# Kernel optimization log

Hardware: AMD Instinct MI355X
Metric: run time of the kernel (lower is better)

## Reference

```python
import jax, jax.numpy as jnp
import numpy as np

N = 100000
E = 3200000

def spmm(edge_row, edge_col, edge_val, support):
    # out[i] = sum_{(i,j) in edges} w_ij * support[j]
    gathered = support[edge_col] * edge_val[:, None]  # [E, F]
    return jax.ops.segment_sum(gathered, edge_row, num_segments=N)

def setup_inputs() -> dict:
    key = jax.random.key(0)
    ks = jax.random.split(key, 10)
    x = jax.random.normal(ks[0], (N, 512), dtype=jnp.float32)
    edge_row = jax.random.randint(ks[1], (E,), 0, N, dtype=jnp.int32)
    edge_col = jax.random.randint(ks[2], (E,), 0, N, dtype=jnp.int32)
    edge_val = jax.random.uniform(ks[3], (E,), dtype=jnp.float32) / 32.0  # ~normalized adj
    def glorot_like(k, shape):
        stdv = 1.0 / np.sqrt(shape[-1])
        return jax.random.uniform(k, shape, dtype=jnp.float32, minval=-stdv, maxval=stdv)
    W1 = glorot_like(ks[4], (512, 256)); b1 = glorot_like(ks[5], (256,))
    W2 = glorot_like(ks[6], (256, 256)); b2 = glorot_like(ks[7], (256,))
    W3 = glorot_like(ks[8], (256, 64)); b3 = glorot_like(ks[9], (64,))
    return {"x": x, "edge_row": edge_row, "edge_col": edge_col, "edge_val": edge_val,
            "W1": W1, "b1": b1, "W2": W2, "b2": b2, "W3": W3, "b3": b3}

def reference(x, edge_row, edge_col, edge_val, W1, b1, W2, b2, W3, b3):
    # layer 1: mm + spmm + bias + relu
    h = spmm(edge_row, edge_col, edge_val, x @ W1) + b1
    h = jax.nn.relu(h)
    # hidden layer (layer_num=3 -> one hidden GraphConvolution); dropout is inference no-op
    h = spmm(edge_row, edge_col, edge_val, h @ W2) + b2
    h = jax.nn.relu(h)
    # output layer
    h = spmm(edge_row, edge_col, edge_val, h @ W3) + b3
    # task='nodecls', ppi=False
    return jax.nn.log_softmax(h, axis=1)
```

## Files before the change

kernel.cpp:

```cpp
#include <hip/hip_runtime.h>
#include <stdint.h>
#include <stddef.h>

typedef __bf16 bf16x8 __attribute__((ext_vector_type(8)));
typedef float  f32x4  __attribute__((ext_vector_type(4)));
typedef float  f32x2  __attribute__((ext_vector_type(2)));

static __device__ __forceinline__ float bf2f(unsigned short u) {
    union { unsigned int i; float f; } v; v.i = ((unsigned int)u) << 16; return v.f;
}
static __device__ __forceinline__ unsigned short f2bf(float f) {
    union { float f; unsigned int i; } v; v.f = f;
    unsigned int r = v.i + 0x7FFFu + ((v.i >> 16) & 1u);
    return (unsigned short)(r >> 16);
}
static __device__ __forceinline__ unsigned cvt_pk_bf16(float a, float b) {
    unsigned r;
    asm volatile("v_cvt_pk_bf16_f32 %0, %1, %2" : "=v"(r) : "v"(a), "v"(b));
    return r;
}
static __device__ __forceinline__ unsigned char f2fp8(float f) {
    return (unsigned char)(__builtin_amdgcn_cvt_pk_fp8_f32(f, f, 0, false) & 0xFF);
}

#define N_NODES 100000
#define N_EDGES 3200000
#define MPAD    100096
#define NB      782
#define NBLK    256
#define EB      (N_EDGES / NBLK)
#define COLMASK 0xFFFFF


__global__ __launch_bounds__(256) void bucket_hist(const int* __restrict__ er, int* __restrict__ blockCnt) {
    __shared__ int h[NB];
    for (int i = threadIdx.x; i < NB; i += 256) h[i] = 0;
    __syncthreads();
    int base = blockIdx.x * EB;
    for (int e = base + threadIdx.x; e < base + EB; e += 256)
        atomicAdd(&h[er[e] >> 7], 1);
    __syncthreads();
    for (int i = threadIdx.x; i < NB; i += 256) blockCnt[blockIdx.x * NB + i] = h[i];
}

__global__ __launch_bounds__(256) void bucket_scan_a(const int* __restrict__ blockCnt,
                                                     int* __restrict__ blockOff,
                                                     int* __restrict__ bucketTotal) {
    __shared__ int s[256];
    int b = blockIdx.x, t = threadIdx.x;
    int v = blockCnt[t * NB + b];
    s[t] = v; __syncthreads();
    for (int off = 1; off < 256; off <<= 1) {
        int u = (t >= off) ? s[t - off] : 0;
        __syncthreads();
        s[t] += u;
        __syncthreads();
    }
    blockOff[t * NB + b] = s[t] - v;
    if (t == 255) bucketTotal[b] = s[255];
}

__global__ __launch_bounds__(1024) void bucket_scan_b(const int* __restrict__ bucketTotal,
                                                      int* __restrict__ bucketStart,
                                                      int* __restrict__ rp, int E,
                                                      int2* __restrict__ cpad) {
    __shared__ int s[1024];
    int t = threadIdx.x;
    int v = (t < NB) ? bucketTotal[t] : 0;
    s[t] = v; __syncthreads();
    for (int off = 1; off < 1024; off <<= 1) {
        int u = (t >= off) ? s[t - off] : 0;
        __syncthreads();
        s[t] += u;
        __syncthreads();
    }
    if (t < NB) bucketStart[t] = s[t] - v;
    if (t == 0) {
        bucketStart[NB] = E; rp[N_NODES] = E;
        for (int i = 0; i < 16; i++) cpad[i] = make_int2(0, 0);
    }
}

__global__ __launch_bounds__(1024) void bucket_scatter(const int* __restrict__ er, const int* __restrict__ ec,
                                                       const float* __restrict__ ev,
                                                       const int* __restrict__ blkCnt,
                                                       const int* __restrict__ blockOff,
                                                       const int* __restrict__ bucketStart,
                                                       int2* __restrict__ cpackT) {
    __shared__ int2 buf[EB];
    __shared__ int  s[1024];
    __shared__ int  scanB[NB];
    __shared__ int  cur[NB];
    int t = threadIdx.x;
    int v = (t < NB) ? blkCnt[blockIdx.x * NB + t] : 0;
    s[t] = v; __syncthreads();
    for (int off = 1; off < 1024; off <<= 1) {
        int u = (t >= off) ? s[t - off] : 0;
        __syncthreads();
        s[t] += u;
        __syncthreads();
    }
    if (t < NB) { scanB[t] = s[t] - v; cur[t] = s[t] - v; }
    __syncthreads();
    int base = blockIdx.x * EB;
    for (int e = base + t; e < base + EB; e += 1024) {
        int r = er[e];
        int p = atomicAdd(&cur[r >> 7], 1);
        buf[p] = make_int2(((r & 127) << 20) | ec[e], __float_as_int(ev[e]));
    }
    __syncthreads();
    for (int i = t; i < EB; i += 1024) {
        int lo = 0, hi = NB - 1;
        while (lo < hi) { int mid = (lo + hi) >> 1; if (cur[mid] <= i) lo = mid + 1; else hi = mid; }
        int gpos = bucketStart[lo] + blockOff[blockIdx.x * NB + lo] + (i - scanB[lo]);
        cpackT[gpos] = buf[i];
    }
}

__global__ __launch_bounds__(256) void bucket_sort(const int2* __restrict__ cpackT,
                                                   const int* __restrict__ bucketStart,
                                                   int2* __restrict__ cpack, int* __restrict__ rp) {
    __shared__ int cnt[128];
    __shared__ int cursor[128];
    int b = blockIdx.x, t = threadIdx.x;
    int s = bucketStart[b], e = bucketStart[b + 1];
    if (t < 128) cnt[t] = 0;
    __syncthreads();
    for (int j = s + t; j < e; j += 256)
        atomicAdd(&cnt[cpackT[j].x >> 20], 1);
    __syncthreads();
    int val = (t < 128) ? cnt[t] : 0;
    for (int off = 1; off < 128; off <<= 1) {
        int u = (t < 128 && t >= off) ? cnt[t - off] : 0;
        __syncthreads();
        if (t < 128) cnt[t] += u;
        __syncthreads();
    }
    if (t < 128) {
        int excl = cnt[t] - val;
        cursor[t] = s + excl;
        int gr = b * 128 + t;
        if (gr < N_NODES) rp[gr] = s + excl;
    }
    __syncthreads();
    for (int j = s + t; j < e; j += 256) {
        int2 v = cpackT[j];
        int p = atomicAdd(&cursor[v.x >> 20], 1);
        cpack[p] = make_int2((v.x & COLMASK) << 8, v.y);
    }
}

__global__ __launch_bounds__(256) void transpose_all(const float* __restrict__ W1, unsigned short* __restrict__ Wt1,
                                                     const float* __restrict__ W2, unsigned short* __restrict__ Wt2,
                                                     const float* __restrict__ W3, unsigned short* __restrict__ Wt3) {
    int i = blockIdx.x * 256 + threadIdx.x;
    const int S1 = 512 * 256, S2 = 256 * 256, S3 = 256 * 64;
    if (i < S1) {
        int k = i / 256, n = i % 256;
        Wt1[(size_t)n * 512 + k] = f2bf(W1[i]);
    } else if (i < S1 + S2) {
        int j = i - S1; int k = j / 256, n = j % 256;
        Wt2[(size_t)n * 256 + k] = f2bf(W2[j]);
    } else if (i < S1 + S2 + S3) {
        int j = i - S1 - S2; int k = j / 64, n = j % 64;
        Wt3[(size_t)n * 256 + k] = f2bf(W3[j]);
    }
}

template<int BM, int BN, int BK, int WROWS, int WCOLS, bool A_F32, int OUT>
__global__ __launch_bounds__(WROWS* WCOLS * 64) void gemm_mfma(const void* __restrict__ Aptr,
                                                 const unsigned short* __restrict__ Bt,
                                                 void* __restrict__ Cptr,
                                                 int K, int Nc, int Mclamp) {
    constexpr int THREADS = WROWS * WCOLS * 64;
    constexpr int WM = BM / WROWS, WN = BN / WCOLS;
    constexpr int MT = WM / 16, NT = WN / 16;
    constexpr int LDA = BK + 8;
    constexpr int KV = BK / 8;

    __shared__ unsigned short lds_a[BM * LDA];
    __shared__ unsigned short lds_b[BN * LDA];

    const int tid  = threadIdx.x;
    const int wid  = tid >> 6, lane = tid & 63;
    const int wrow = wid / WCOLS, wcol = wid % WCOLS;
    const int bm = blockIdx.x * BM, bn = blockIdx.y * BN;
    const int r = lane & 15, q = lane >> 4;

    const float*          Af = (const float*)Aptr;
    const unsigned short* Ab = (const unsigned short*)Aptr;

    f32x4 acc[MT][NT];
    f32x4 zero = {0.f, 0.f, 0.f, 0.f};
#pragma unroll
    for (int mi = 0; mi < MT; mi++)
#pragma unroll
        for (int ni = 0; ni < NT; ni++) acc[mi][ni] = zero;

    for (int k0 = 0; k0 < K; k0 += BK) {
#pragma unroll
        for (int it = 0; it < (BM * KV) / THREADS; it++) {
            int v = tid + it * THREADS;
            int row = v / KV, kc = (v % KV) * 8;
            int grow = bm + row;
            uint4 d;
            if constexpr (A_F32) {
                grow = (grow <= Mclamp) ? grow : Mclamp;
                const float4* pp = (const float4*)(Af + (size_t)grow * K + k0 + kc);
                float4 f0 = pp[0], f1 = pp[1];
                d.x = cvt_pk_bf16(f0.x, f0.y);
                d.y = cvt_pk_bf16(f0.z, f0.w);
                d.z = cvt_pk_bf16(f1.x, f1.y);
                d.w = cvt_pk_bf16(f1.z, f1.w);
            } else {
                d = *(const uint4*)(Ab + (size_t)grow * K + k0 + kc);
            }
            *(uint4*)&lds_a[row * LDA + kc] = d;
        }
#pragma unroll
        for (int it = 0; it < (BN * KV) / THREADS; it++) {
            int v = tid + it * THREADS;
            int row = v / KV, kc = (v % KV) * 8;
            uint4 d = *(const uint4*)(Bt + (size_t)(bn + row) * K + k0 + kc);
            *(uint4*)&lds_b[row * LDA + kc] = d;
        }
        __syncthreads();

#pragma unroll
        for (int kk = 0; kk < BK; kk += 32) {
            bf16x8 av[MT], bv[NT];
#pragma unroll
            for (int mi = 0; mi < MT; mi++)
                av[mi] = *(const bf16x8*)&lds_a[(wrow * WM + mi * 16 + r) * LDA + kk + q * 8];
#pragma unroll
            for (int ni = 0; ni < NT; ni++)
                bv[ni] = *(const bf16x8*)&lds_b[(wcol * WN + ni * 16 + r) * LDA + kk + q * 8];
#pragma unroll
            for (int mi = 0; mi < MT; mi++)
#pragma unroll
                for (int ni = 0; ni < NT; ni++)
                    acc[mi][ni] = __builtin_amdgcn_mfma_f32_16x16x32_bf16(av[mi], bv[ni], acc[mi][ni], 0, 0, 0);
        }
        __syncthreads();
    }

#pragma unroll
    for (int mi = 0; mi < MT; mi++) {
        int row = bm + wrow * WM + mi * 16 + q * 4;
#pragma unroll
        for (int ni = 0; ni < NT; ni++) {
            int cc = bn + wcol * WN + ni * 16 + r;
#pragma unroll
            for (int d = 0; d < 4; d++) {
                if constexpr (OUT == 0) {
                    ((unsigned short*)Cptr)[(size_t)(row + d) * Nc + cc] = f2bf(acc[mi][ni][d]);
                } else {
                    ((unsigned char*)Cptr)[(size_t)(row + d) * Nc + cc] = f2fp8(acc[mi][ni][d]);
                }
            }
        }
    }
}

__global__ __launch_bounds__(256) void spmm_f256_fp8(const int* __restrict__ rp, const int2* __restrict__ cpack,
                                                     const unsigned char* __restrict__ Z8,
                                                     const float* __restrict__ bias, unsigned short* __restrict__ H, int N) {
    int w = __builtin_amdgcn_readfirstlane((int)((blockIdx.x * 256 + threadIdx.x) >> 6));
    if (w >= N) return;
    int lane = threadIdx.x & 63;
    int f4 = lane * 4;
    int s = __builtin_amdgcn_readfirstlane(rp[w]);
    int e = __builtin_amdgcn_readfirstlane(rp[w + 1]);
    f32x2 acc01 = {0.f, 0.f}, acc23 = {0.f, 0.f};
    int j = s;

#define EDGE_BLK(UN, MASKED) { \
        int2 eb[UN]; \
        _Pragma("unroll") \
        for (int t = 0; t < UN; t++) eb[t] = cpack[j + t]; \
        _Pragma("unroll") \
        for (int t = 0; t < UN; t++) { \
            int ex = __builtin_amdgcn_readfirstlane(eb[t].x); \
            int ew = __builtin_amdgcn_readfirstlane(eb[t].y); \
            if (MASKED) ew = (j + t < e) ? ew : 0; \
            float wt = __int_as_float(ew); \
            unsigned z = *(const unsigned*)(Z8 + (size_t)(unsigned)ex + f4); \
            f32x2 lo = __builtin_amdgcn_cvt_pk_f32_fp8((int)z, false); \
            f32x2 hi = __builtin_amdgcn_cvt_pk_f32_fp8((int)z, true);  \
            f32x2 wv = {wt, wt}; \
            acc01 += wv * lo; \
            acc23 += wv * hi; \
        } }

    for (; j + 16 <= e; j += 16) EDGE_BLK(16, false)
    for (; j < e; j += 8)        EDGE_BLK(8,  true)
#undef EDGE_BLK

    float4 b = *(const float4*)(bias + f4);
    float a0 = fmaxf(acc01.x + b.x, 0.f), a1 = fmaxf(acc01.y + b.y, 0.f);
    float a2 = fmaxf(acc23.x + b.z, 0.f), a3 = fmaxf(acc23.y + b.w, 0.f);
    ushort4 o; o.x = f2bf(a0); o.y = f2bf(a1); o.z = f2bf(a2); o.w = f2bf(a3);
    *(ushort4*)(H + (size_t)w * 256 + f4) = o;
}

__global__ __launch_bounds__(256) void spmm_f64_lsm(const int* __restrict__ rp, const int2* __restrict__ cpack,
                                                    const unsigned short* __restrict__ Z,
                                                    const float* __restrict__ bias, float* __restrict__ out, int N) {
    int w = __builtin_amdgcn_readfirstlane((int)((blockIdx.x * 256 + threadIdx.x) >> 6));
    if (w >= N) return;
    int lane = threadIdx.x & 63;
    const unsigned char* Zb = (const unsigned char*)Z;
    int s = __builtin_amdgcn_readfirstlane(rp[w]);
    int e = __builtin_amdgcn_readfirstlane(rp[w + 1]);
    float acc = 0.f;
    int j = s;

#define EDGE_BLK(UN, MASKED) { \
        int2 eb[UN]; \
        _Pragma("unroll") \
        for (int t = 0; t < UN; t++) eb[t] = cpack[j + t]; \
        _Pragma("unroll") \
        for (int t = 0; t < UN; t++) { \
            int ex = __builtin_amdgcn_readfirstlane(eb[t].x); \
            int ew = __builtin_amdgcn_readfirstlane(eb[t].y); \
            if (MASKED) ew = (j + t < e) ? ew : 0; \
            float wt = __int_as_float(ew); \
             \
            unsigned short z = *(const unsigned short*)(Zb + (size_t)(unsigned)(ex >> 1) + lane * 2); \
            acc += wt * bf2f(z); \
        } }

    for (; j + 8 <= e; j += 8) EDGE_BLK(8, false)
    for (; j < e; j += 4)      EDGE_BLK(4, true)
#undef EDGE_BLK

    float a = acc + bias[lane];
    float m = a;
#pragma unroll
    for (int off = 32; off >= 1; off >>= 1) m = fmaxf(m, __shfl_xor(m, off, 64));
    float p = __expf(a - m);
    float sum = p;
#pragma unroll
    for (int off = 32; off >= 1; off >>= 1) sum += __shfl_xor(sum, off, 64);
    out[(size_t)w * 64 + lane] = a - m - __logf(sum);
}

extern "C" void kernel_launch(void* const* d_in, const int* in_sizes, int n_in,
                              void* d_out, int out_size, void* d_ws, size_t ws_size,
                              hipStream_t stream) {
    const float* x  = (const float*)d_in[0];
    const int*   er = (const int*)  d_in[1];
    const int*   ec = (const int*)  d_in[2];
    const float* ev = (const float*)d_in[3];
    const float* W1 = (const float*)d_in[4];
    const float* b1 = (const float*)d_in[5];
    const float* W2 = (const float*)d_in[6];
    const float* b2 = (const float*)d_in[7];
    const float* W3 = (const float*)d_in[8];
    const float* b3 = (const float*)d_in[9];

    const int N = N_NODES, E = N_EDGES;

    char* p = (char*)d_ws;
    auto alloc = [&](size_t bytes) -> char* {
        char* q = p; p += (bytes + 255) & ~(size_t)255; return q;
    };
    unsigned short* Wt1    = (unsigned short*)alloc((size_t)256 * 512 * 2);
    unsigned short* Wt2    = (unsigned short*)alloc((size_t)256 * 256 * 2);
    unsigned short* Wt3    = (unsigned short*)alloc((size_t)64  * 256 * 2);
    int*            rp     = (int*)  alloc((size_t)(N + 1) * 4);
    int*            blkCnt = (int*)  alloc((size_t)NBLK * NB * 4);
    int*            blkOff = (int*)  alloc((size_t)NBLK * NB * 4);
    int*            bktTot = (int*)  alloc((size_t)NB * 4);
    int*            bktSt  = (int*)  alloc((size_t)(NB + 1) * 4);
    int2*           cpack  = (int2*) alloc((size_t)(E + 16) * 8);
    unsigned char*  Z8     = (unsigned char*) alloc((size_t)MPAD * 256);
    unsigned short* bufA   = (unsigned short*)alloc((size_t)MPAD * 256 * 2);
    unsigned short* bufB   = (unsigned short*)alloc((size_t)MPAD * 256 * 2);
    int2*           cpackT = (int2*)bufA;

    bucket_hist   <<<NBLK, 256, 0, stream>>>(er, blkCnt);
    bucket_scan_a <<<NB,   256, 0, stream>>>(blkCnt, blkOff, bktTot);
    bucket_scan_b <<<1,   1024, 0, stream>>>(bktTot, bktSt, rp, E, cpack + E);
    bucket_scatter<<<NBLK, 1024, 0, stream>>>(er, ec, ev, blkCnt, blkOff, bktSt, cpackT);
    bucket_sort   <<<NB,   256, 0, stream>>>(cpackT, bktSt, cpack, rp);

    transpose_all<<<(512*256 + 256*256 + 256*64 + 255) / 256, 256, 0, stream>>>(W1, Wt1, W2, Wt2, W3, Wt3);

    gemm_mfma<128, 128, 64, 4, 2, true , 1><<<dim3(MPAD / 128, 2), 512, 0, stream>>>(x,    Wt1, Z8,   512, 256, N - 1);
    spmm_f256_fp8<<<N / 4, 256, 0, stream>>>(rp, cpack, Z8, b1, bufB, N);
    gemm_mfma<128, 128, 64, 4, 2, false, 1><<<dim3(MPAD / 128, 2), 512, 0, stream>>>(bufB, Wt2, Z8,   256, 256, N - 1);
    spmm_f256_fp8<<<N / 4, 256, 0, stream>>>(rp, cpack, Z8, b2, bufB, N);
    gemm_mfma<128, 64, 64, 4, 2, false, 0><<<dim3(MPAD / 128, 1), 512, 0, stream>>>(bufB, Wt3, bufA, 256, 64, N - 1);
    spmm_f64_lsm<<<N / 4, 256, 0, stream>>>(rp, cpack, bufA, b3, (float*)d_out, N);
}
```

Measured before the change: 788.6 us.

## Register-prefetch next GEMM tile during MFMA and widen SpMM edge unroll

```diff
diff --git a/kernel.cpp b/kernel.cpp
--- a/kernel.cpp
+++ b/kernel.cpp
@@ -177,6 +177,8 @@
     constexpr int MT = WM / 16, NT = WN / 16;
     constexpr int LDA = BK + 8;
     constexpr int KV = BK / 8;
+    constexpr int A_ITERS = (BM * KV) / THREADS;
+    constexpr int B_ITERS = (BN * KV) / THREADS;
 
     __shared__ unsigned short lds_a[BM * LDA];
     __shared__ unsigned short lds_b[BN * LDA];
@@ -197,35 +199,58 @@
 #pragma unroll
         for (int ni = 0; ni < NT; ni++) acc[mi][ni] = zero;
 
-    for (int k0 = 0; k0 < K; k0 += BK) {
-#pragma unroll
-        for (int it = 0; it < (BM * KV) / THREADS; it++) {
+    float4 raf[A_ITERS][2];
+    uint4  rab[A_ITERS];
+    uint4  rb[B_ITERS];
+
+    auto load_tile = [&](int k0) {
+#pragma unroll
+        for (int it = 0; it < A_ITERS; it++) {
             int v = tid + it * THREADS;
             int row = v / KV, kc = (v % KV) * 8;
             int grow = bm + row;
-            uint4 d;
             if constexpr (A_F32) {
                 grow = (grow <= Mclamp) ? grow : Mclamp;
                 const float4* pp = (const float4*)(Af + (size_t)grow * K + k0 + kc);
-                float4 f0 = pp[0], f1 = pp[1];
-                d.x = cvt_pk_bf16(f0.x, f0.y);
-                d.y = cvt_pk_bf16(f0.z, f0.w);
-                d.z = cvt_pk_bf16(f1.x, f1.y);
-                d.w = cvt_pk_bf16(f1.z, f1.w);
+                raf[it][0] = pp[0];
+                raf[it][1] = pp[1];
             } else {
-                d = *(const uint4*)(Ab + (size_t)grow * K + k0 + kc);
+                rab[it] = *(const uint4*)(Ab + (size_t)grow * K + k0 + kc);
+            }
+        }
+#pragma unroll
+        for (int it = 0; it < B_ITERS; it++) {
+            int v = tid + it * THREADS;
+            int row = v / KV, kc = (v % KV) * 8;
+            rb[it] = *(const uint4*)(Bt + (size_t)(bn + row) * K + k0 + kc);
+        }
+    };
+
+    auto write_lds = [&]() {
+#pragma unroll
+        for (int it = 0; it < A_ITERS; it++) {
+            int v = tid + it * THREADS;
+            int row = v / KV, kc = (v % KV) * 8;
+            uint4 d;
+            if constexpr (A_F32) {
+                d.x = cvt_pk_bf16(raf[it][0].x, raf[it][0].y);
+                d.y = cvt_pk_bf16(raf[it][0].z, raf[it][0].w);
+                d.z = cvt_pk_bf16(raf[it][1].x, raf[it][1].y);
+                d.w = cvt_pk_bf16(raf[it][1].z, raf[it][1].w);
+            } else {
+                d = rab[it];
             }
             *(uint4*)&lds_a[row * LDA + kc] = d;
         }
 #pragma unroll
-        for (int it = 0; it < (BN * KV) / THREADS; it++) {
+        for (int it = 0; it < B_ITERS; it++) {
             int v = tid + it * THREADS;
             int row = v / KV, kc = (v % KV) * 8;
-            uint4 d = *(const uint4*)(Bt + (size_t)(bn + row) * K + k0 + kc);
-            *(uint4*)&lds_b[row * LDA + kc] = d;
-        }
-        __syncthreads();
-
+            *(uint4*)&lds_b[row * LDA + kc] = rb[it];
+        }
+    };
+
+    auto compute = [&]() {
 #pragma unroll
         for (int kk = 0; kk < BK; kk += 32) {
             bf16x8 av[MT], bv[NT];
@@ -241,8 +266,19 @@
                 for (int ni = 0; ni < NT; ni++)
                     acc[mi][ni] = __builtin_amdgcn_mfma_f32_16x16x32_bf16(av[mi], bv[ni], acc[mi][ni], 0, 0, 0);
         }
-        __syncthreads();
-    }
+    };
+
+    load_tile(0);
+    write_lds();
+    __syncthreads();
+    for (int k0 = BK; k0 < K; k0 += BK) {
+        load_tile(k0);
+        compute();
+        __syncthreads();
+        write_lds();
+        __syncthreads();
+    }
+    compute();
 
 #pragma unroll
     for (int mi = 0; mi < MT; mi++) {
@@ -292,7 +328,7 @@
             acc23 += wv * hi; \
         } }
 
-    for (; j + 16 <= e; j += 16) EDGE_BLK(16, false)
+    for (; j + 32 <= e; j += 32) EDGE_BLK(32, false)
     for (; j < e; j += 8)        EDGE_BLK(8,  true)
 #undef EDGE_BLK
 
@@ -330,8 +366,8 @@
             acc += wt * bf2f(z); \
         } }
 
-    for (; j + 8 <= e; j += 8) EDGE_BLK(8, false)
-    for (; j < e; j += 4)      EDGE_BLK(4, true)
+    for (; j + 16 <= e; j += 16) EDGE_BLK(16, false)
+    for (; j < e; j += 4)        EDGE_BLK(4, true)
 #undef EDGE_BLK
 
     float a = acc + bias[lane];
```

After: 893.9 us. 13.4% more time.

## Load GEMM tiles directly into LDS with XOR-swizzled layout

Applied to the files above, without the earlier changes.

```diff
diff --git a/kernel.cpp b/kernel.cpp
--- a/kernel.cpp
+++ b/kernel.cpp
@@ -21,6 +21,11 @@
 }
 static __device__ __forceinline__ unsigned char f2fp8(float f) {
     return (unsigned char)(__builtin_amdgcn_cvt_pk_fp8_f32(f, f, 0, false) & 0xFF);
+}
+static __device__ __forceinline__ void gload_lds16(const void* g, void* l) {
+    __builtin_amdgcn_global_load_lds(
+        (const __attribute__((address_space(1))) unsigned int*)g,
+        (__attribute__((address_space(3))) unsigned int*)l, 16, 0, 0);
 }
 
 #define N_NODES 100000
@@ -175,11 +180,12 @@
     constexpr int THREADS = WROWS * WCOLS * 64;
     constexpr int WM = BM / WROWS, WN = BN / WCOLS;
     constexpr int MT = WM / 16, NT = WN / 16;
-    constexpr int LDA = BK + 8;
     constexpr int KV = BK / 8;
-
-    __shared__ unsigned short lds_a[BM * LDA];
-    __shared__ unsigned short lds_b[BN * LDA];
+    constexpr int A_ITERS = (BM * KV) / THREADS;
+    constexpr int B_ITERS = (BN * KV) / THREADS;
+
+    __shared__ unsigned short lds_a[BM * BK];
+    __shared__ unsigned short lds_b[BN * BK];
 
     const int tid  = threadIdx.x;
     const int wid  = tid >> 6, lane = tid & 63;
@@ -199,42 +205,49 @@
 
     for (int k0 = 0; k0 < K; k0 += BK) {
 #pragma unroll
-        for (int it = 0; it < (BM * KV) / THREADS; it++) {
+        for (int it = 0; it < B_ITERS; it++) {
             int v = tid + it * THREADS;
-            int row = v / KV, kc = (v % KV) * 8;
-            int grow = bm + row;
-            uint4 d;
+            int row = v / KV, qc = v % KV;
+            int qs = qc ^ (row & 7);
+            gload_lds16(Bt + (size_t)(bn + row) * K + k0 + qs * 8, &lds_b[v * 8]);
+        }
+#pragma unroll
+        for (int it = 0; it < A_ITERS; it++) {
+            int v = tid + it * THREADS;
+            int row = v / KV, qc = v % KV;
             if constexpr (A_F32) {
+                int grow = bm + row;
                 grow = (grow <= Mclamp) ? grow : Mclamp;
-                const float4* pp = (const float4*)(Af + (size_t)grow * K + k0 + kc);
+                const float4* pp = (const float4*)(Af + (size_t)grow * K + k0 + qc * 8);
                 float4 f0 = pp[0], f1 = pp[1];
+                uint4 d;
                 d.x = cvt_pk_bf16(f0.x, f0.y);
                 d.y = cvt_pk_bf16(f0.z, f0.w);
                 d.z = cvt_pk_bf16(f1.x, f1.y);
                 d.w = cvt_pk_bf16(f1.z, f1.w);
+                *(uint4*)&lds_a[row * BK + (qc ^ (row & 7)) * 8] = d;
             } else {
-                d = *(const uint4*)(Ab + (size_t)grow * K + k0 + kc);
+                int qs = qc ^ (row & 7);
+                gload_lds16(Ab + (size_t)(bm + row) * K + k0 + qs * 8, &lds_a[v * 8]);
             }
-            *(uint4*)&lds_a[row * LDA + kc] = d;
         }
-#pragma unroll
-        for (int it = 0; it < (BN * KV) / THREADS; it++) {
-            int v = tid + it * THREADS;
-            int row = v / KV, kc = (v % KV) * 8;
-            uint4 d = *(const uint4*)(Bt + (size_t)(bn + row) * K + k0 + kc);
-            *(uint4*)&lds_b[row * LDA + kc] = d;
-        }
         __syncthreads();
 
 #pragma unroll
         for (int kk = 0; kk < BK; kk += 32) {
+#pragma unroll
+            for (int dummy = 0; dummy < 1; dummy++) {}
             bf16x8 av[MT], bv[NT];
 #pragma unroll
-            for (int mi = 0; mi < MT; mi++)
-                av[mi] = *(const bf16x8*)&lds_a[(wrow * WM + mi * 16 + r) * LDA + kk + q * 8];
-#pragma unroll
-            for (int ni = 0; ni < NT; ni++)
-                bv[ni] = *(const bf16x8*)&lds_b[(wcol * WN + ni * 16 + r) * LDA + kk + q * 8];
+            for (int mi = 0; mi < MT; mi++) {
+                int arow = wrow * WM + mi * 16 + r;
+                av[mi] = *(const bf16x8*)&lds_a[arow * BK + ((kk / 8 + q) ^ (arow & 7)) * 8];
+            }
+#pragma unroll
+            for (int ni = 0; ni < NT; ni++) {
+                int brow = wcol * WN + ni * 16 + r;
+                bv[ni] = *(const bf16x8*)&lds_b[brow * BK + ((kk / 8 + q) ^ (brow & 7)) * 8];
+            }
 #pragma unroll
             for (int mi = 0; mi < MT; mi++)
 #pragma unroll
```

Result: no change. 775.6 us (-1.6%).
